# Kernel optimization log

Measured on AMD Instinct MI355X. Metric: run time of the kernel, lower is better.

The kernel has to match this reference:

```python
import jax, jax.numpy as jnp
import numpy as np

N_SRC, N_MID, N_OUT = 100000, 20000, 5000
E1, E2 = 20000, 20000
IN, H, EF = 64, 64, 32


def setup_inputs() -> dict:
    key = jax.random.key(0)
    ks = jax.random.split(key, 12)
    s = 1.0 / np.sqrt(EF)
    return {
        "in_feat": jax.random.normal(ks[0], (N_SRC, IN), jnp.float32),
        "edge_feats": jax.random.normal(ks[1], (E1, EF), jnp.float32),
        "edge_feats1": jax.random.normal(ks[2], (E2, EF), jnp.float32),
        "W1": jax.random.uniform(ks[3], (EF, IN * H), jnp.float32, -s, s),
        "b1": jax.random.uniform(ks[4], (IN * H,), jnp.float32, -s, s),
        "W2": jax.random.uniform(ks[5], (EF, H * H), jnp.float32, -s, s),
        "b2": jax.random.uniform(ks[6], (H * H,), jnp.float32, -s, s),
        "src1": jax.random.randint(ks[7], (E1,), 0, N_SRC, jnp.int32),
        "dst1": jax.random.randint(ks[8], (E1,), 0, N_MID, jnp.int32),
        "src2": jax.random.randint(ks[9], (E2,), 0, N_MID, jnp.int32),
        "dst2": jax.random.randint(ks[10], (E2,), 0, N_OUT, jnp.int32),
    }


def nnconv_mean(h, efeat, W, b, src, dst, n_dst, d_in, d_out):
    # per-edge weight matrix from edge MLP: [E, d_in, d_out]
    We = (efeat @ W + b).reshape(-1, d_in, d_out)
    # gather src feats and apply per-edge matmul: [E, d_out]
    msg = jnp.einsum("ei,eio->eo", h[src], We)
    # scatter-mean into dst nodes (empty dst -> 0, matching DGL mean)
    sums = jax.ops.segment_sum(msg, dst, num_segments=n_dst)
    cnt = jax.ops.segment_sum(jnp.ones((dst.shape[0],), msg.dtype), dst,
                              num_segments=n_dst)
    return sums / jnp.maximum(cnt, 1.0)[:, None]


def reference(in_feat, edge_feats, edge_feats1, W1, b1, W2, b2,
              src1, dst1, src2, dst2):
    h = nnconv_mean(in_feat, edge_feats, W1, b1, src1, dst1, N_MID, IN, H)
    h = jax.nn.relu(h)
    h = nnconv_mean(h, edge_feats1, W2, b2, src2, dst2, N_OUT, H, H)
    return h
```

## Files before the change

kernel.cpp:

```cpp
#include <hip/hip_runtime.h>
#include <hip/hip_bf16.h>

#define N_SRC 100000
#define N_MID 20000
#define N_OUT 5000
#define E_1   20000
#define E_2   20000
#define NCHUNK 33
#define NSPLIT 4
#define NBLK   313
#define EPAD   (NBLK*64)
#define MAXDEG 32

typedef float f32x4 __attribute__((ext_vector_type(4)));
typedef short s16x8 __attribute__((ext_vector_type(8)));

__device__ __forceinline__ void load_lds16(const void* g, void* l) {
    __builtin_amdgcn_global_load_lds(
        (const __attribute__((address_space(1))) unsigned int*)g,
        (__attribute__((address_space(3))) unsigned int*)l, 16, 0, 0);
}

__device__ __forceinline__ s16x8 pack_bf16x8(float4 x, float4 y, float s) {
    union { s16x8 v; __hip_bfloat162 h[4]; } u;
    u.h[0] = __float22bfloat162_rn(make_float2(s * x.x, s * x.y));
    u.h[1] = __float22bfloat162_rn(make_float2(s * x.z, s * x.w));
    u.h[2] = __float22bfloat162_rn(make_float2(s * y.x, s * y.y));
    u.h[3] = __float22bfloat162_rn(make_float2(s * y.z, s * y.w));
    return u.v;
}

__device__ __forceinline__ unsigned short f2bf_rne(float f) {
    unsigned u = __float_as_uint(f);
    return (unsigned short)((u + 0x7FFFu + ((u >> 16) & 1u)) >> 16);
}

__global__ void prep_kernel(const float* __restrict__ W1, const float* __restrict__ b1,
                            const float* __restrict__ W2, const float* __restrict__ b2,
                            uint4* __restrict__ Wt1, uint4* __restrict__ Wt2)
{
    int gid = blockIdx.x * 256 + threadIdx.x;
    if (gid >= 2 * NCHUNK * 512) return;
    int layer = gid / (NCHUNK * 512);
    int r     = gid % (NCHUNK * 512);
    int c  = r / 512;
    int u  = r % 512;
    int k8 = u / 64;
    int n  = u % 64;
    const float* W = layer ? W2 : W1;
    const float* b = layer ? b2 : b1;
    const float* s = (c < 32) ? (W + (size_t)c * 4096) : b;
    union { uint4 v; unsigned short us[8]; } pk;
    #pragma unroll
    for (int j = 0; j < 8; ++j)
        pk.us[j] = f2bf_rne(s[(k8 * 8 + j) * 64 + n]);
    uint4* Wt = layer ? Wt2 : Wt1;
    Wt[(size_t)c * 512 + n * 8 + (k8 ^ (n & 7))] = pk.v;
}

__global__ void count_slot_kernel(const int* __restrict__ dst1, const int* __restrict__ dst2,
                                  int* __restrict__ cur1, int* __restrict__ slots1,
                                  int* __restrict__ cur2, int* __restrict__ slots2)
{
    int i = blockIdx.x * blockDim.x + threadIdx.x;
    if (i < E_1) {
        int d = dst1[i];
        int p = atomicAdd(&cur1[d], 1);
        if (p < MAXDEG) slots1[(size_t)d * MAXDEG + p] = i;
    } else if (i < E_1 + E_2) {
        int e = i - E_1;
        int d = dst2[e];
        int p = atomicAdd(&cur2[d], 1);
        if (p < MAXDEG) slots2[(size_t)d * MAXDEG + p] = e;
    }
}

__global__ __launch_bounds__(256) void nnconv_mfma(
    const float* __restrict__ h,
    const float* __restrict__ efeat,
    const uint4* __restrict__ Wt,
    const int*  __restrict__ src,
    int E,
    float* __restrict__ msg)
{
    __shared__ float efs[64][9];
    __shared__ uint4 wbuf[2][512];

    const int t  = threadIdx.x;
    const int w  = t >> 6;
    const int l  = t & 63;
    const int m15 = l & 15;
    const int q   = l >> 4;
    const int ebase = blockIdx.x * 64;
    const int split = blockIdx.y;
    const int c_lo = (split == 0) ? 0 : (split * 8 + 1);
    const int c_hi = split * 8 + 9;
    const int nc   = c_hi - c_lo;

    for (int idx = t; idx < 64 * nc; idx += 256) {
        int e = idx / nc, j = idx - e * nc;
        int eg = ebase + e, f = c_lo + j;
        float v = 0.0f;
        if (eg < E) v = (f < 32) ? efeat[eg * 32 + f] : 1.0f;
        efs[e][j] = v;
    }

    {
        const uint4* g = Wt + (size_t)c_lo * 512;
        load_lds16(g + t,       &wbuf[0][t]);
        load_lds16(g + 256 + t, &wbuf[0][256 + t]);
    }

    const int e_a = ebase + w * 16 + m15;
    const int row = (e_a < E) ? src[e_a] : 0;
    const float* hp = h + (size_t)row * 64 + q * 8;
    const float4 ha0 = *(const float4*)(hp);
    const float4 ha1 = *(const float4*)(hp + 4);
    const float4 hb0 = *(const float4*)(hp + 32);
    const float4 hb1 = *(const float4*)(hp + 36);

    f32x4 acc[4] = {};
    const int nx = m15 & 7;

    int cur = 0;
    for (int c = c_lo; c < c_hi; ++c) {
        __syncthreads();
        if (c + 1 < c_hi) {
            const uint4* g = Wt + (size_t)(c + 1) * 512;
            load_lds16(g + t,       &wbuf[cur ^ 1][t]);
            load_lds16(g + 256 + t, &wbuf[cur ^ 1][256 + t]);
        }
        const float ef = efs[w * 16 + m15][c - c_lo];
        const s16x8 a0 = pack_bf16x8(ha0, ha1, ef);
        const s16x8 a1 = pack_bf16x8(hb0, hb1, ef);
        const uint4* wb = wbuf[cur];
        #pragma unroll
        for (int c16 = 0; c16 < 4; ++c16) {
            const int n = c16 * 16 + m15;
            const s16x8 b0 = *(const s16x8*)&wb[n * 8 + ((q)     ^ nx)];
            const s16x8 b1 = *(const s16x8*)&wb[n * 8 + ((4 + q) ^ nx)];
            acc[c16] = __builtin_amdgcn_mfma_f32_16x16x32_bf16(a0, b0, acc[c16], 0, 0, 0);
            acc[c16] = __builtin_amdgcn_mfma_f32_16x16x32_bf16(a1, b1, acc[c16], 0, 0, 0);
        }
        cur ^= 1;
    }

    float* mp = msg + (size_t)split * EPAD * 64;
    #pragma unroll
    for (int r = 0; r < 4; ++r) {
        float* rp = mp + (size_t)(ebase + w * 16 + q * 4 + r) * 64 + m15;
        #pragma unroll
        for (int c16 = 0; c16 < 4; ++c16)
            rp[c16 * 16] = acc[c16][r];
    }
}

__global__ void gather_mean(const float* __restrict__ msg,
                            const int* __restrict__ slots, const int* __restrict__ cur,
                            int n_dst, int do_relu, float* __restrict__ outp)
{
    int d = blockIdx.x * 4 + (threadIdx.x >> 6);
    int o = threadIdx.x & 63;
    if (d >= n_dst) return;
    int deg = cur[d];
    int dg = min(deg, MAXDEG);
    float s = 0.0f;
    for (int j = 0; j < dg; ++j) {
        int e = slots[(size_t)d * MAXDEG + j];
        const float* mrow = msg + (size_t)e * 64 + o;
        #pragma unroll
        for (int sp = 0; sp < NSPLIT; ++sp)
            s += mrow[(size_t)sp * EPAD * 64];
    }
    s *= 1.0f / fmaxf((float)deg, 1.0f);
    if (do_relu) s = fmaxf(s, 0.0f);
    outp[(size_t)d * 64 + o] = s;
}

extern "C" void kernel_launch(void* const* d_in, const int* in_sizes, int n_in,
                              void* d_out, int out_size, void* d_ws, size_t ws_size,
                              hipStream_t stream)
{
    const float* in_feat = (const float*)d_in[0];
    const float* ef1     = (const float*)d_in[1];
    const float* ef2     = (const float*)d_in[2];
    const float* W1      = (const float*)d_in[3];
    const float* b1      = (const float*)d_in[4];
    const float* W2      = (const float*)d_in[5];
    const float* b2      = (const float*)d_in[6];
    const int*   src1    = (const int*)d_in[7];
    const int*   dst1    = (const int*)d_in[8];
    const int*   src2    = (const int*)d_in[9];
    const int*   dst2    = (const int*)d_in[10];

    float* h_mid  = (float*)d_ws;
    int*   cur1   = (int*)(h_mid + (size_t)N_MID * 64);
    int*   cur2   = cur1 + N_MID;
    int*   slots1 = cur2 + N_OUT;
    int*   slots2 = slots1 + (size_t)N_MID * MAXDEG;
    uint4* Wt1    = (uint4*)(slots2 + (size_t)N_OUT * MAXDEG);
    uint4* Wt2    = Wt1 + (size_t)NCHUNK * 512;
    float* msg    = (float*)(Wt2 + (size_t)NCHUNK * 512);
    float* out    = (float*)d_out;

    hipMemsetAsync(cur1, 0, (size_t)(N_MID + N_OUT) * sizeof(int), stream);

    prep_kernel<<<(2 * NCHUNK * 512 + 255) / 256, 256, 0, stream>>>(W1, b1, W2, b2, Wt1, Wt2);
    count_slot_kernel<<<(E_1 + E_2 + 255) / 256, 256, 0, stream>>>(dst1, dst2,
                                                                   cur1, slots1, cur2, slots2);

    dim3 grid(NBLK, NSPLIT);
    nnconv_mfma<<<grid, 256, 0, stream>>>(in_feat, ef1, Wt1, src1, E_1, msg);
    gather_mean<<<(N_MID + 3) / 4, 256, 0, stream>>>(msg, slots1, cur1, N_MID, 1, h_mid);

    nnconv_mfma<<<grid, 256, 0, stream>>>(h_mid, ef2, Wt2, src2, E_2, msg);
    gather_mean<<<(N_OUT + 3) / 4, 256, 0, stream>>>(msg, slots2, cur2, N_OUT, 0, out);
}
```

Measured before the change: 146.4 us.

## Process 128 edges per block with shared weight fragments and merge setup kernels

```diff
diff --git a/kernel.cpp b/kernel.cpp
--- a/kernel.cpp
+++ b/kernel.cpp
@@ -7,10 +7,15 @@
 #define E_1   20000
 #define E_2   20000
 #define NCHUNK 33
-#define NSPLIT 4
-#define NBLK   313
-#define EPAD   (NBLK*64)
+#define NSPLIT 5
+#define EBLK   128
+#define NBLK   157
+#define EPAD   (NBLK*EBLK)
 #define MAXDEG 32
+
+#define PREP_N      (2*NCHUNK*512)
+#define PREP_BLKS   ((PREP_N + 255)/256)
+#define COUNT_BLKS  ((E_1 + E_2 + 255)/256)
 
 typedef float f32x4 __attribute__((ext_vector_type(4)));
 typedef short s16x8 __attribute__((ext_vector_type(8)));
@@ -35,43 +40,44 @@
     return (unsigned short)((u + 0x7FFFu + ((u >> 16) & 1u)) >> 16);
 }
 
-__global__ void prep_kernel(const float* __restrict__ W1, const float* __restrict__ b1,
-                            const float* __restrict__ W2, const float* __restrict__ b2,
-                            uint4* __restrict__ Wt1, uint4* __restrict__ Wt2)
-{
-    int gid = blockIdx.x * 256 + threadIdx.x;
-    if (gid >= 2 * NCHUNK * 512) return;
-    int layer = gid / (NCHUNK * 512);
-    int r     = gid % (NCHUNK * 512);
-    int c  = r / 512;
-    int u  = r % 512;
-    int k8 = u / 64;
-    int n  = u % 64;
-    const float* W = layer ? W2 : W1;
-    const float* b = layer ? b2 : b1;
-    const float* s = (c < 32) ? (W + (size_t)c * 4096) : b;
-    union { uint4 v; unsigned short us[8]; } pk;
-    #pragma unroll
-    for (int j = 0; j < 8; ++j)
-        pk.us[j] = f2bf_rne(s[(k8 * 8 + j) * 64 + n]);
-    uint4* Wt = layer ? Wt2 : Wt1;
-    Wt[(size_t)c * 512 + n * 8 + (k8 ^ (n & 7))] = pk.v;
-}
-
-__global__ void count_slot_kernel(const int* __restrict__ dst1, const int* __restrict__ dst2,
-                                  int* __restrict__ cur1, int* __restrict__ slots1,
-                                  int* __restrict__ cur2, int* __restrict__ slots2)
-{
-    int i = blockIdx.x * blockDim.x + threadIdx.x;
-    if (i < E_1) {
-        int d = dst1[i];
-        int p = atomicAdd(&cur1[d], 1);
-        if (p < MAXDEG) slots1[(size_t)d * MAXDEG + p] = i;
-    } else if (i < E_1 + E_2) {
-        int e = i - E_1;
-        int d = dst2[e];
-        int p = atomicAdd(&cur2[d], 1);
-        if (p < MAXDEG) slots2[(size_t)d * MAXDEG + p] = e;
+__global__ __launch_bounds__(256) void setup_kernel(
+    const float* __restrict__ W1, const float* __restrict__ b1,
+    const float* __restrict__ W2, const float* __restrict__ b2,
+    uint4* __restrict__ Wt1, uint4* __restrict__ Wt2,
+    const int* __restrict__ dst1, const int* __restrict__ dst2,
+    int* __restrict__ cur1, int* __restrict__ slots1,
+    int* __restrict__ cur2, int* __restrict__ slots2)
+{
+    if (blockIdx.x < PREP_BLKS) {
+        int gid = blockIdx.x * 256 + threadIdx.x;
+        if (gid >= PREP_N) return;
+        int layer = gid / (NCHUNK * 512);
+        int r     = gid % (NCHUNK * 512);
+        int c  = r / 512;
+        int u  = r % 512;
+        int k8 = u / 64;
+        int n  = u % 64;
+        const float* W = layer ? W2 : W1;
+        const float* b = layer ? b2 : b1;
+        const float* s = (c < 32) ? (W + (size_t)c * 4096) : b;
+        union { uint4 v; unsigned short us[8]; } pk;
+        #pragma unroll
+        for (int j = 0; j < 8; ++j)
+            pk.us[j] = f2bf_rne(s[(k8 * 8 + j) * 64 + n]);
+        uint4* Wt = layer ? Wt2 : Wt1;
+        Wt[(size_t)c * 512 + n * 8 + (k8 ^ (n & 7))] = pk.v;
+    } else {
+        int i = (blockIdx.x - PREP_BLKS) * 256 + threadIdx.x;
+        if (i < E_1) {
+            int d = dst1[i];
+            int p = atomicAdd(&cur1[d], 1);
+            if (p < MAXDEG) slots1[(size_t)d * MAXDEG + p] = i;
+        } else if (i < E_1 + E_2) {
+            int e = i - E_1;
+            int d = dst2[e];
+            int p = atomicAdd(&cur2[d], 1);
+            if (p < MAXDEG) slots2[(size_t)d * MAXDEG + p] = e;
+        }
     }
 }
 
@@ -83,7 +89,7 @@
     int E,
     float* __restrict__ msg)
 {
-    __shared__ float efs[64][9];
+    __shared__ float efs[7][EBLK];
     __shared__ uint4 wbuf[2][512];
 
     const int t  = threadIdx.x;
@@ -91,18 +97,18 @@
     const int l  = t & 63;
     const int m15 = l & 15;
     const int q   = l >> 4;
-    const int ebase = blockIdx.x * 64;
+    const int ebase = blockIdx.x * EBLK;
     const int split = blockIdx.y;
-    const int c_lo = (split == 0) ? 0 : (split * 8 + 1);
-    const int c_hi = split * 8 + 9;
+    const int c_lo = (split * 33) / NSPLIT;
+    const int c_hi = ((split + 1) * 33) / NSPLIT;
     const int nc   = c_hi - c_lo;
 
-    for (int idx = t; idx < 64 * nc; idx += 256) {
-        int e = idx / nc, j = idx - e * nc;
-        int eg = ebase + e, f = c_lo + j;
+    for (int idx = t; idx < nc * EBLK; idx += 256) {
+        int f = idx >> 7, e = idx & (EBLK - 1);
+        int eg = ebase + e, c = c_lo + f;
         float v = 0.0f;
-        if (eg < E) v = (f < 32) ? efeat[eg * 32 + f] : 1.0f;
-        efs[e][j] = v;
+        if (eg < E) v = (c < 32) ? efeat[eg * 32 + c] : 1.0f;
+        efs[f][e] = v;
     }
 
     {
@@ -111,15 +117,23 @@
         load_lds16(g + 256 + t, &wbuf[0][256 + t]);
     }
 
-    const int e_a = ebase + w * 16 + m15;
-    const int row = (e_a < E) ? src[e_a] : 0;
-    const float* hp = h + (size_t)row * 64 + q * 8;
-    const float4 ha0 = *(const float4*)(hp);
-    const float4 ha1 = *(const float4*)(hp + 4);
-    const float4 hb0 = *(const float4*)(hp + 32);
-    const float4 hb1 = *(const float4*)(hp + 36);
-
-    f32x4 acc[4] = {};
+    const int e0 = ebase + w * 32 + m15;
+    const int e1 = e0 + 16;
+    const int r0 = (e0 < E) ? src[e0] : 0;
+    const int r1 = (e1 < E) ? src[e1] : 0;
+    const float* hp0 = h + (size_t)r0 * 64 + q * 8;
+    const float* hp1 = h + (size_t)r1 * 64 + q * 8;
+    const float4 t0a0 = *(const float4*)(hp0);
+    const float4 t0a1 = *(const float4*)(hp0 + 4);
+    const float4 t0b0 = *(const float4*)(hp0 + 32);
+    const float4 t0b1 = *(const float4*)(hp0 + 36);
+    const float4 t1a0 = *(const float4*)(hp1);
+    const float4 t1a1 = *(const float4*)(hp1 + 4);
+    const float4 t1b0 = *(const float4*)(hp1 + 32);
+    const float4 t1b1 = *(const float4*)(hp1 + 36);
+
+    f32x4 acc0[4] = {};
+    f32x4 acc1[4] = {};
     const int nx = m15 & 7;
 
     int cur = 0;
@@ -130,17 +144,22 @@
             load_lds16(g + t,       &wbuf[cur ^ 1][t]);
             load_lds16(g + 256 + t, &wbuf[cur ^ 1][256 + t]);
         }
-        const float ef = efs[w * 16 + m15][c - c_lo];
-        const s16x8 a0 = pack_bf16x8(ha0, ha1, ef);
-        const s16x8 a1 = pack_bf16x8(hb0, hb1, ef);
+        const float ef0 = efs[c - c_lo][w * 32 + m15];
+        const float ef1 = efs[c - c_lo][w * 32 + 16 + m15];
+        const s16x8 a00 = pack_bf16x8(t0a0, t0a1, ef0);
+        const s16x8 a01 = pack_bf16x8(t0b0, t0b1, ef0);
+        const s16x8 a10 = pack_bf16x8(t1a0, t1a1, ef1);
+        const s16x8 a11 = pack_bf16x8(t1b0, t1b1, ef1);
         const uint4* wb = wbuf[cur];
         #pragma unroll
-        for (int c16 = 0; c16 < 4; ++c16) {
-            const int n = c16 * 16 + m15;
+        for (int n16 = 0; n16 < 4; ++n16) {
+            const int n = n16 * 16 + m15;
             const s16x8 b0 = *(const s16x8*)&wb[n * 8 + ((q)     ^ nx)];
             const s16x8 b1 = *(const s16x8*)&wb[n * 8 + ((4 + q) ^ nx)];
-            acc[c16] = __builtin_amdgcn_mfma_f32_16x16x32_bf16(a0, b0, acc[c16], 0, 0, 0);
-            acc[c16] = __builtin_amdgcn_mfma_f32_16x16x32_bf16(a1, b1, acc[c16], 0, 0, 0);
+            acc0[n16] = __builtin_amdgcn_mfma_f32_16x16x32_bf16(a00, b0, acc0[n16], 0, 0, 0);
+            acc0[n16] = __builtin_amdgcn_mfma_f32_16x16x32_bf16(a01, b1, acc0[n16], 0, 0, 0);
+            acc1[n16] = __builtin_amdgcn_mfma_f32_16x16x32_bf16(a10, b0, acc1[n16], 0, 0, 0);
+            acc1[n16] = __builtin_amdgcn_mfma_f32_16x16x32_bf16(a11, b1, acc1[n16], 0, 0, 0);
         }
         cur ^= 1;
     }
@@ -148,16 +167,20 @@
     float* mp = msg + (size_t)split * EPAD * 64;
     #pragma unroll
     for (int r = 0; r < 4; ++r) {
-        float* rp = mp + (size_t)(ebase + w * 16 + q * 4 + r) * 64 + m15;
-        #pragma unroll
-        for (int c16 = 0; c16 < 4; ++c16)
-            rp[c16 * 16] = acc[c16][r];
-    }
-}
-
-__global__ void gather_mean(const float* __restrict__ msg,
-                            const int* __restrict__ slots, const int* __restrict__ cur,
-                            int n_dst, int do_relu, float* __restrict__ outp)
+        float* rp0 = mp + (size_t)(ebase + w * 32 + q * 4 + r) * 64 + m15;
+        float* rp1 = rp0 + 16 * 64;
+        #pragma unroll
+        for (int n16 = 0; n16 < 4; ++n16) {
+            rp0[n16 * 16] = acc0[n16][r];
+            rp1[n16 * 16] = acc1[n16][r];
+        }
+    }
+}
+
+__global__ __launch_bounds__(256) void gather_mean(
+    const float* __restrict__ msg,
+    const int* __restrict__ slots, const int* __restrict__ cur,
+    int n_dst, int do_relu, float* __restrict__ outp)
 {
     int d = blockIdx.x * 4 + (threadIdx.x >> 6);
     int o = threadIdx.x & 63;
@@ -205,9 +228,8 @@
 
     hipMemsetAsync(cur1, 0, (size_t)(N_MID + N_OUT) * sizeof(int), stream);
 
-    prep_kernel<<<(2 * NCHUNK * 512 + 255) / 256, 256, 0, stream>>>(W1, b1, W2, b2, Wt1, Wt2);
-    count_slot_kernel<<<(E_1 + E_2 + 255) / 256, 256, 0, stream>>>(dst1, dst2,
-                                                                   cur1, slots1, cur2, slots2);
+    setup_kernel<<<PREP_BLKS + COUNT_BLKS, 256, 0, stream>>>(
+        W1, b1, W2, b2, Wt1, Wt2, dst1, dst2, cur1, slots1, cur2, slots2);
 
     dim3 grid(NBLK, NSPLIT);
     nnconv_mfma<<<grid, 256, 0, stream>>>(in_feat, ef1, Wt1, src1, E_1, msg);
```

Result: slower. 159.0 us (+8.6%).
